# Kernel tuning notes

Hardware: AMD Instinct MI355X
Metric: run time of the kernel (lower is better)

The kernel has to match this reference:

```python
import jax, jax.numpy as jnp
import numpy as np

NUM_CELLS = 15        # num_beams (polar bins over (-pi/2, pi/2])
NEIGH = 2.0           # neighborhood_size -> default fallback radius
P, B = 2048, 10000    # pedestrians, boundary points
EMB, HDIM, MID, BOT = 64, 64, 512, 1024


def setup_inputs() -> dict:
    key = jax.random.key(0)
    ks = jax.random.split(key, 8)
    def n(k, shp, s=1.0):
        return jax.random.normal(k, shp, dtype=jnp.float32) * s
    return {
        "h_states": n(ks[0], (1, P, HDIM)),
        "end_pos": n(ks[1], (P, 2), 4.0),
        "rel_pos": n(ks[2], (P, 2)),
        "boundary_points": n(ks[3], (B, 2), 5.0),
        "W_sp": n(ks[4], (2, EMB), 0.5),
        "b_sp": jnp.zeros((EMB,), jnp.float32),
        "W1": n(ks[5], (EMB + HDIM, MID), 0.05),
        "b1": jnp.zeros((MID,), jnp.float32),
        "g1": jnp.ones((MID,), jnp.float32),
        "be1": jnp.zeros((MID,), jnp.float32),
        "W2": n(ks[6], (MID, BOT), 0.05),
        "b2": jnp.zeros((BOT,), jnp.float32),
        "g2": jnp.ones((BOT,), jnp.float32),
        "be2": jnp.zeros((BOT,), jnp.float32),
    }


def _bn(x, g, b, eps=1e-5):
    # torch BatchNorm1d in training mode: biased batch statistics
    m = x.mean(axis=0)
    v = x.var(axis=0)
    return g * (x - m) * jax.lax.rsqrt(v + eps) + b


def _polar_grid(end_pos, rel_pos, bpts, nb, radius):
    # Vectorized replacement of the pandas pd.cut + groupby(...).idxmin path.
    Pn, Bn = end_pos.shape[0], bpts.shape[0]
    th_ped = jnp.arctan2(rel_pos[:, 1], rel_pos[:, 0])      # (P,)
    c, s = jnp.cos(th_ped)[:, None], jnp.sin(th_ped)[:, None]
    d = bpts[None, :, :] - end_pos[:, None, :]              # (P,B,2)
    xb = d[..., 0] * c + d[..., 1] * s                      # rotate into ped frame
    yb = -d[..., 0] * s + d[..., 1] * c
    r = jnp.sqrt(xb * xb + yb * yb)                         # (P,B)
    th = jnp.arctan2(yb, xb)                                # (P,B)

    width = np.pi / nb
    binid = jnp.clip(jnp.floor((th + np.pi / 2) / width).astype(jnp.int32), 0, nb - 1)
    valid = (th > -np.pi / 2) & (th <= np.pi / 2)           # pd.cut: (a, b] intervals
    pid = jnp.arange(Pn, dtype=jnp.int32)[:, None]
    dump = Pn * nb                                          # segment for out-of-range points
    seg = jnp.where(valid, pid * nb + binid, dump)          # (P,B)

    # appended fallback rows: one per (ped, bin) at bin-center angle, radius=neighborhood_size
    centers = jnp.linspace(-np.pi / 2 + np.pi / nb / 2,
                           np.pi / 2 - np.pi / nb / 2, nb).astype(jnp.float32)
    r_all = jnp.concatenate([r.ravel(), jnp.full((Pn * nb,), radius, jnp.float32)])
    th_all = jnp.concatenate([th.ravel(), jnp.tile(centers, Pn)])
    seg_all = jnp.concatenate([seg.ravel(), jnp.arange(Pn * nb, dtype=jnp.int32)])

    ns = Pn * nb + 1
    rmin = jax.ops.segment_min(r_all, seg_all, num_segments=ns)
    # argmin with first-occurrence tie-break (matches pandas idxmin ordering)
    N = r_all.shape[0]
    idx = jnp.arange(N, dtype=jnp.int32)
    cand = jnp.where(r_all <= rmin[seg_all], idx, N)
    arg = jax.ops.segment_min(cand, seg_all, num_segments=ns)[:Pn * nb]

    th_ch = th_all[arg].reshape(Pn, nb)
    r_ch = rmin[:Pn * nb].reshape(Pn, nb)
    xc = r_ch * jnp.cos(th_ch)
    yc = r_ch * jnp.sin(th_ch)
    # rotate back to world frame and translate
    x = xc * c - yc * s + end_pos[:, 0:1]
    y = xc * s + yc * c + end_pos[:, 1:2]
    return jnp.stack([x, y], axis=-1)                       # (P, nb, 2)


def reference(h_states, end_pos, rel_pos, boundary_points,
              W_sp, b_sp, W1, b1, g1, be1, W2, b2, g2, be2):
    cart = _polar_grid(end_pos, rel_pos, boundary_points, NUM_CELLS, NEIGH)
    rel_grid = (cart - end_pos[:, None, :]).reshape(-1, 2)  # (P*nb, 2)
    emb = rel_grid @ W_sp + b_sp                            # spatial_embedding
    h = h_states.reshape(-1, HDIM)                          # (P, h_dim)
    hid = jnp.repeat(h, NUM_CELLS, axis=0)                  # R1,R1,...,R2,R2,...
    x = jnp.concatenate([emb, hid], axis=1)                 # (P*nb, 128)
    x = jax.nn.relu(_bn(x @ W1 + b1, g1, be1))
    x = jax.nn.relu(_bn(x @ W2 + b2, g2, be2))
    return x.reshape(P, NUM_CELLS, BOT).max(axis=1)         # (P, bottleneck_dim)
```

## Files before the change

### kernel.cpp

```cpp
#include <hip/hip_runtime.h>
#include <hip/hip_bf16.h>
#include <math.h>

#define P_N   2048
#define B_N   10000
#define NB    15
#define MROWS (P_N * NB)
#define SPLIT 5
#define BPB   (B_N / SPLIT)

typedef __bf16 bf16x8 __attribute__((ext_vector_type(8)));
typedef float  f32x4  __attribute__((ext_vector_type(4)));

__device__ __forceinline__ float bf2f(unsigned short u) {
    union { unsigned int i; float f; } v; v.i = ((unsigned int)u) << 16; return v.f;
}
__device__ __forceinline__ unsigned short f2bf(float f) {
    union { float f; unsigned int i; } v; v.f = f;
    unsigned int i = v.i;
    i += 0x7FFFu + ((i >> 16) & 1u);
    return (unsigned short)(i >> 16);
}
__device__ __forceinline__ void gld_lds16(const unsigned short* g, unsigned short* l) {
    __builtin_amdgcn_global_load_lds(
        (const __attribute__((address_space(1))) unsigned int*)g,
        (__attribute__((address_space(3))) unsigned int*)l, 16, 0, 0);
}
__device__ __forceinline__ unsigned fkey(float f) {
    unsigned b = __float_as_uint(f);
    return (b & 0x80000000u) ? ~b : (b | 0x80000000u);
}
__device__ __forceinline__ float funkey(unsigned key) {
    unsigned b = (key & 0x80000000u) ? (key ^ 0x80000000u) : ~key;
    return __uint_as_float(b);
}

__global__ __launch_bounds__(256) void k_front(const float* __restrict__ W1,
        const float* __restrict__ W2, unsigned short* __restrict__ w1t,
        unsigned short* __restrict__ w2t, float* __restrict__ stats,
        const float* __restrict__ end_pos, const float* __restrict__ rel_pos,
        const float* __restrict__ bpts, unsigned long long* __restrict__ pkeys,
        const float* __restrict__ h, unsigned short* __restrict__ hbf,
        const float* __restrict__ Wsp, const float* __restrict__ bsp,
        const float* __restrict__ b1, float* __restrict__ V0,
        float* __restrict__ V1, float* __restrict__ cvec) {
    __shared__ unsigned short t[64][65];
    __shared__ unsigned long long s_key[NB];
    int blk = blockIdx.x, tid = threadIdx.x;
    if (blk < 144) {
        const float* W; unsigned short* O; int NC, K, tr, tc;
        if (blk < 16) { W = W1; O = w1t; NC = 512; K = 128; tr = blk & 1; tc = blk >> 1; }
        else { int b = blk - 16; W = W2; O = w2t; NC = 1024; K = 512; tr = b & 7; tc = b >> 3; }
        int r0 = tr * 64, c0 = tc * 64;
        int cx = tid & 63, rg = tid >> 6;
#pragma unroll
        for (int i = 0; i < 16; ++i) {
            int r = rg * 16 + i;
            t[r][cx] = f2bf(W[(size_t)(r0 + r) * NC + c0 + cx]);
        }
        __syncthreads();
#pragma unroll
        for (int i = 0; i < 16; ++i) {
            int n = rg * 16 + i;
            O[(size_t)(c0 + n) * K + r0 + cx] = t[cx][n];
        }
    } else if (blk < 2196) {
        int zidx = (blk - 144) * 256 + tid;
        if (zidx < 525056) {
            uint4 z = {0u, 0u, 0u, 0u};
            ((uint4*)stats)[zidx] = z;
        }
    } else if (blk < 2198) {
        int col = (blk - 2196) * 256 + tid;
        float v0 = 0.f, v1 = 0.f, cc = 0.f;
        for (int e = 0; e < 64; ++e) {
            float w = W1[(size_t)e * 512 + col];
            v0 = fmaf(Wsp[e], w, v0);
            v1 = fmaf(Wsp[64 + e], w, v1);
            cc = fmaf(bsp[e], w, cc);
        }
        V0[col] = v0; V1[col] = v1; cvec[col] = cc + b1[col];
    } else if (blk < 2326) {
        int base = (blk - 2198) * 1024 + tid * 4;
        float4 hv = *(const float4*)(h + base);
        unsigned short ub[4] = {f2bf(hv.x), f2bf(hv.y), f2bf(hv.z), f2bf(hv.w)};
        *(uint2*)(hbf + base) = *(uint2*)ub;
    } else {
        int sb = blk - 2326;
        int p = sb / SPLIT, part = sb % SPLIT;
        if (tid < NB) s_key[tid] = ~0ull;
        __syncthreads();

        float ex = end_pos[2 * p], ey = end_pos[2 * p + 1];
        float rx = rel_pos[2 * p], ry = rel_pos[2 * p + 1];
        float rr = rx * rx + ry * ry;
        float c, s;
        if (rr > 0.0f) { float inv = 1.0f / sqrtf(rr); c = rx * inv; s = ry * inv; }
        else           { c = 1.0f; s = 0.0f; }

        const float T0 = -4.704630109f, T1 = -2.246036774f, T2 = -1.376381920f,
                    T3 = -0.900404044f, T4 = -0.577350269f, T5 = -0.324919696f,
                    T6 = -0.105104235f, T7 =  0.105104235f, T8 =  0.324919696f,
                    T9 =  0.577350269f, T10 = 0.900404044f, T11 = 1.376381920f,
                    T12 = 2.246036774f, T13 = 4.704630109f;

        const float2* bp2 = (const float2*)bpts;
        int bstart = part * BPB;
        for (int b = bstart + tid; b < bstart + BPB; b += 256) {
            float2 pt = bp2[b];
            float dx = pt.x - ex, dy = pt.y - ey;
            float xb = dx * c + dy * s;
            float yb = dy * c - dx * s;
            float r2 = xb * xb + yb * yb;
            bool v3 = yb > T7 * xb;
            float ta = v3 ? T11 : T3;
            bool v2 = yb > ta * xb;
            float tb = v3 ? (v2 ? T13 : T9) : (v2 ? T5 : T1);
            bool v1 = yb > tb * xb;
            float tc = v3 ? (v2 ? (v1 ? 3.0e38f : T12) : (v1 ? T10 : T8))
                          : (v2 ? (v1 ? T6 : T4)       : (v1 ? T2 : T0));
            bool v0 = yb > tc * xb;
            int bin = (v3 ? 8 : 0) + (v2 ? 4 : 0) + (v1 ? 2 : 0) + (v0 ? 1 : 0);
            if (xb > 0.0f) {
                unsigned long long key =
                    ((unsigned long long)__float_as_uint(r2) << 32) | (unsigned int)b;
                atomicMin(&s_key[bin], key);
            }
        }
        __syncthreads();
        if (tid < NB) pkeys[(size_t)part * MROWS + p * NB + tid] = s_key[tid];
    }
}

__global__ __launch_bounds__(64) void k_assemble(
        const unsigned long long* __restrict__ pkeys,
        const float* __restrict__ end_pos, const float* __restrict__ rel_pos,
        const float* __restrict__ bpts, float* __restrict__ rel,
        float* __restrict__ pm0, float* __restrict__ pm1, float* __restrict__ pm2,
        float* __restrict__ pm3, float* __restrict__ pm4) {
    int p = blockIdx.x, tid = threadIdx.x;
    float relx = 0.f, rely = 0.f;
    if (tid < NB) {
        float ex = end_pos[2 * p], ey = end_pos[2 * p + 1];
        unsigned long long key = ~0ull;
#pragma unroll
        for (int part = 0; part < SPLIT; ++part) {
            unsigned long long k = pkeys[(size_t)part * MROWS + p * NB + tid];
            key = (k < key) ? k : key;
        }
        float r = sqrtf(__uint_as_float((unsigned int)(key >> 32)));
        if (r <= 2.0f) {
            int b = (int)(key & 0xFFFFFFFFu);
            relx = bpts[2 * b] - ex; rely = bpts[2 * b + 1] - ey;
        } else {
            float rx = rel_pos[2 * p], ry = rel_pos[2 * p + 1];
            float rr = rx * rx + ry * ry;
            float c, s;
            if (rr > 0.0f) { float inv = 1.0f / sqrtf(rr); c = rx * inv; s = ry * inv; }
            else           { c = 1.0f; s = 0.0f; }
            float th = ((float)tid + 0.5f) * (float)(M_PI / 15.0) - (float)(M_PI / 2.0);
            float xc = 2.0f * cosf(th), yc = 2.0f * sinf(th);
            relx = xc * c - yc * s;
            rely = xc * s + yc * c;
        }
        rel[(size_t)(p * NB + tid) * 2]     = relx;
        rel[(size_t)(p * NB + tid) * 2 + 1] = rely;
    }
    float m0 = relx, m1 = rely, m2 = relx * relx, m3 = relx * rely, m4 = rely * rely;
#pragma unroll
    for (int d = 32; d >= 1; d >>= 1) {
        m0 += __shfl_xor(m0, d); m1 += __shfl_xor(m1, d);
        m2 += __shfl_xor(m2, d); m3 += __shfl_xor(m3, d);
        m4 += __shfl_xor(m4, d);
    }
    if (tid == 0) { pm0[p] = m0; pm1[p] = m1; pm2[p] = m2; pm3[p] = m3; pm4[p] = m4; }
}

__global__ __launch_bounds__(512) void k_hgemm(const unsigned short* __restrict__ hbf,
        const unsigned short* __restrict__ w1t, float* __restrict__ Hp,
        const float* __restrict__ V0, const float* __restrict__ V1,
        const float* __restrict__ cvec,
        const float* __restrict__ pm0, const float* __restrict__ pm1,
        const float* __restrict__ pm2, const float* __restrict__ pm3,
        const float* __restrict__ pm4,
        float* __restrict__ s1, float* __restrict__ q1) {
    __shared__ __align__(16) unsigned short lds[24576];
    int tid = threadIdx.x;
    int bm = blockIdx.x & 15, bnn = blockIdx.x >> 4;
    int row0 = bm << 7, col0 = bnn << 8;
    int lane = tid & 63, wave = tid >> 6;
    int wr = wave >> 2, wc = wave & 3;
    int frow = lane & 15, kq = lane >> 4;

    f32x4 zero = {0.f, 0.f, 0.f, 0.f};
    f32x4 acc[4][4];
#pragma unroll
    for (int i = 0; i < 4; ++i)
#pragma unroll
        for (int j = 0; j < 4; ++j) acc[i][j] = zero;

#pragma unroll
    for (int k = 0; k < 6; ++k) {
        int ch = wave * 6 + k;
        int s = (ch >= 24) ? 1 : 0;
        int r = ch - s * 24;
        unsigned short* dst = lds + s * 12288 + r * 512;
        const unsigned short* src =
            (r < 8) ? (hbf + (size_t)(row0 + r * 16 + frow) * 64 + s * 32 + kq * 8)
                    : (w1t + (size_t)(col0 + (r - 8) * 16 + frow) * 128 + 64 + s * 32 + kq * 8);
        gld_lds16(src, dst);
    }
    asm volatile("s_waitcnt vmcnt(0)" ::: "memory");
    __builtin_amdgcn_s_barrier();
    asm volatile("" ::: "memory");

#pragma unroll
    for (int s = 0; s < 2; ++s) {
        const unsigned short* sub = lds + s * 12288;
        bf16x8 af[4], bfv[4];
#pragma unroll
        for (int i = 0; i < 4; ++i)
            af[i] = *(const bf16x8*)&sub[(wr * 4 + i) * 512 + kq * 128 + frow * 8];
#pragma unroll
        for (int j = 0; j < 4; ++j)
            bfv[j] = *(const bf16x8*)&sub[4096 + (wc * 4 + j) * 512 + kq * 128 + frow * 8];
#pragma unroll
        for (int i = 0; i < 4; ++i)
#pragma unroll
            for (int j = 0; j < 4; ++j)
                acc[i][j] = __builtin_amdgcn_mfma_f32_16x16x32_bf16(af[i], bfv[j], acc[i][j], 0, 0, 0);
    }

    float v0c[4], v1c[4], cc[4];
#pragma unroll
    for (int j = 0; j < 4; ++j) {
        int col = col0 + wc * 64 + j * 16 + frow;
        v0c[j] = V0[col]; v1c[j] = V1[col]; cc[j] = cvec[col];
    }
    float csum[4] = {0.f, 0.f, 0.f, 0.f}, csq[4] = {0.f, 0.f, 0.f, 0.f};
#pragma unroll
    for (int i = 0; i < 4; ++i) {
#pragma unroll
        for (int r = 0; r < 4; ++r) {
            int row = row0 + wr * 64 + i * 16 + kq * 4 + r;
            float srx = pm0[row], sry = pm1[row];
            float sxx = pm2[row], sxy = pm3[row], syy = pm4[row];
#pragma unroll
            for (int j = 0; j < 4; ++j) {
                int col = col0 + wc * 64 + j * 16 + frow;
                float hp = acc[i][j][r];
                Hp[(size_t)row * 512 + col] = hp;
                float A  = hp + cc[j];
                float B1 = fmaf(srx, v0c[j], sry * v1c[j]);
                float B2 = fmaf(v0c[j] * v0c[j], sxx,
                           fmaf(2.0f * v0c[j] * v1c[j], sxy, v1c[j] * v1c[j] * syy));
                csum[j] += fmaf(15.0f, A, B1);
                csq[j]  += fmaf(15.0f, A * A, fmaf(2.0f * A, B1, B2));
            }
        }
    }
#pragma unroll
    for (int j = 0; j < 4; ++j) {
        int col = col0 + wc * 64 + j * 16 + frow;
        float cs = csum[j], cq = csq[j];
        cs += __shfl_xor(cs, 16); cs += __shfl_xor(cs, 32);
        cq += __shfl_xor(cq, 16); cq += __shfl_xor(cq, 32);
        if (lane < 16) { atomicAdd(&s1[col], cs); atomicAdd(&q1[col], cq); }
    }
}

__global__ __launch_bounds__(256) void k_y1w(const float* __restrict__ Hp,
        const float* __restrict__ rel, const float* __restrict__ V0,
        const float* __restrict__ V1, const float* __restrict__ cvec,
        const float* __restrict__ s1, const float* __restrict__ q1,
        const float* __restrict__ g1, const float* __restrict__ be1,
        unsigned short* __restrict__ Y1) {
    int tid = threadIdx.x;
    int p = blockIdx.x;
    int seg = tid & 63, cg = tid >> 6;
    const float invN = 1.0f / (float)MROWS;
    float4 ha = *(const float4*)(Hp + (size_t)p * 512 + seg * 8);
    float4 hb = *(const float4*)(Hp + (size_t)p * 512 + seg * 8 + 4);
    float4 ca = *(const float4*)(cvec + seg * 8);
    float4 cb = *(const float4*)(cvec + seg * 8 + 4);
    float4 va = *(const float4*)(V0 + seg * 8), vb = *(const float4*)(V0 + seg * 8 + 4);
    float4 wa = *(const float4*)(V1 + seg * 8), wb = *(const float4*)(V1 + seg * 8 + 4);
    float hc[8] = {ha.x+ca.x, ha.y+ca.y, ha.z+ca.z, ha.w+ca.w,
                   hb.x+cb.x, hb.y+cb.y, hb.z+cb.z, hb.w+cb.w};
    float v0[8] = {va.x,va.y,va.z,va.w,vb.x,vb.y,vb.z,vb.w};
    float v1[8] = {wa.x,wa.y,wa.z,wa.w,wb.x,wb.y,wb.z,wb.w};
    float sc[8], sh[8];
#pragma unroll
    for (int j = 0; j < 8; ++j) {
        int ccix = seg * 8 + j;
        float m = s1[ccix] * invN;
        float v = q1[ccix] * invN - m * m;
        float k = g1[ccix] * rsqrtf(v + 1e-5f);
        sc[j] = k; sh[j] = be1[ccix] - m * k;
    }
#pragma unroll
    for (int i = 0; i < 4; ++i) {
        int cell = cg + i * 4;
        if (cell < NB) {
            float2 rl = *(const float2*)(rel + (size_t)(p * NB + cell) * 2);
            unsigned short ub[8];
#pragma unroll
            for (int j = 0; j < 8; ++j) {
                float y = fmaf(rl.x, v0[j], fmaf(rl.y, v1[j], hc[j]));
                float z = fmaxf(fmaf(y, sc[j], sh[j]), 0.0f);
                ub[j] = f2bf(z);
            }
            *(uint4*)(Y1 + (size_t)(p * NB + cell) * 512 + seg * 8) = *(uint4*)ub;
        }
    }
}

template<int K, bool WRITE_C>
__global__ __launch_bounds__(512) void k_gemm256(
        const unsigned short* __restrict__ A, const unsigned short* __restrict__ Bt,
        const float* __restrict__ bias, unsigned short* __restrict__ C,
        int N, float* __restrict__ osum, float* __restrict__ osq,
        unsigned int* __restrict__ mkey) {
    __shared__ __align__(16) unsigned short lds[65536];
    int tid = threadIdx.x;

    int nbt = N >> 8;
    int d = blockIdx.x;
    int m5 = d >> 3;
    int bn = m5 % nbt;
    int bm = (d & 7) + ((m5 / nbt) << 3);
    int row0 = bm << 8, col0 = bn << 8;

    int lane = tid & 63, wave = tid >> 6;
    int wr = wave >> 2, wc = wave & 3;
    int frow = lane & 15, kq = lane >> 4;

    f32x4 zero = {0.f, 0.f, 0.f, 0.f};
    f32x4 acc[8][4];
#pragma unroll
    for (int i = 0; i < 8; ++i)
#pragma unroll
        for (int j = 0; j < 4; ++j) acc[i][j] = zero;

    const unsigned short* gsrc =
        (wave < 4) ? (A  + (size_t)(row0 + (wave << 6) + frow) * K + kq * 8)
                   : (Bt + (size_t)(col0 + ((wave - 4) << 6) + frow) * K + kq * 8);
    unsigned regbase = (wave < 4) ? (unsigned)wave * 2048
                                  : 8192u + (unsigned)(wave - 4) * 2048;

    auto issue2 = [&](int t, int s, int hp) {
        unsigned short* dst = lds + (t & 1) * 32768 + s * 16384 + regbase + hp * 1024;
        const unsigned short* src = gsrc + t * 64 + s * 32 + (size_t)(hp * 32) * K;
        gld_lds16(src,                  dst);
        gld_lds16(src + (size_t)16 * K, dst + 512);
    };

    constexpr int NT = K / 64;
    static_assert(NT >= 2, "need >=2 K-tiles");

    issue2(0, 0, 0); issue2(0, 0, 1); issue2(0, 1, 0); issue2(0, 1, 1);

#pragma unroll
    for (int t = 0; t < NT; ++t) {
        const unsigned short* buf = lds + (t & 1) * 32768;
        bool more = (t + 1 < NT);
#pragma unroll
        for (int s = 0; s < 2; ++s) {
            const unsigned short* sub = buf + s * 16384;
            if (more || s == 0) asm volatile("s_waitcnt vmcnt(4)" ::: "memory");
            else                asm volatile("s_waitcnt vmcnt(0)" ::: "memory");
            __builtin_amdgcn_s_barrier();
            asm volatile("" ::: "memory");
            bf16x8 bfv[4], af[4];
#pragma unroll
            for (int j = 0; j < 4; ++j)
                bfv[j] = *(const bf16x8*)&sub[8192 + (wc * 4 + j) * 512 + kq * 128 + frow * 8];
#pragma unroll
            for (int i = 0; i < 4; ++i)
                af[i] = *(const bf16x8*)&sub[(wr * 8 + i) * 512 + kq * 128 + frow * 8];
            if (more) issue2(t + 1, s, 0);
            __builtin_amdgcn_s_barrier();
            asm volatile("" ::: "memory");
            __builtin_amdgcn_s_setprio(1);
#pragma unroll
            for (int i = 0; i < 4; ++i)
#pragma unroll
                for (int j = 0; j < 4; ++j)
                    acc[i][j] = __builtin_amdgcn_mfma_f32_16x16x32_bf16(af[i], bfv[j], acc[i][j], 0, 0, 0);
            __builtin_amdgcn_s_setprio(0);
#pragma unroll
            for (int i = 0; i < 4; ++i)
                af[i] = *(const bf16x8*)&sub[(wr * 8 + 4 + i) * 512 + kq * 128 + frow * 8];
            if (more) issue2(t + 1, s, 1);
            __builtin_amdgcn_s_barrier();
            asm volatile("" ::: "memory");
            __builtin_amdgcn_s_setprio(1);
#pragma unroll
            for (int i = 0; i < 4; ++i)
#pragma unroll
                for (int j = 0; j < 4; ++j)
                    acc[4 + i][j] = __builtin_amdgcn_mfma_f32_16x16x32_bf16(af[i], bfv[j], acc[4 + i][j], 0, 0, 0);
            __builtin_amdgcn_s_setprio(0);
        }
    }

    float bv[4];
#pragma unroll
    for (int j = 0; j < 4; ++j) bv[j] = bias[col0 + wc * 64 + j * 16 + frow];

#pragma unroll
    for (int j = 0; j < 4; ++j) {
        int col = col0 + wc * 64 + j * 16 + frow;
        float csum = 0.f, csq = 0.f;
#pragma unroll
        for (int i = 0; i < 8; ++i) {
#pragma unroll
            for (int r = 0; r < 4; ++r) {
                float y = acc[i][j][r] + bv[j];
                csum += y; csq = fmaf(y, y, csq);
            }
        }
        csum += __shfl_xor(csum, 16); csum += __shfl_xor(csum, 32);
        csq  += __shfl_xor(csq, 16);  csq  += __shfl_xor(csq, 32);
        if (lane < 16) { atomicAdd(&osum[col], csum); atomicAdd(&osq[col], csq); }
    }

    unsigned short* ldsC = lds;
#pragma unroll
    for (int b = 0; b < 4; ++b) {
        __syncthreads();
        if (wr == (b >> 1)) {
#pragma unroll
            for (int j = 0; j < 4; ++j) {
#pragma unroll
                for (int ii = 0; ii < 4; ++ii) {
                    int i = (b & 1) * 4 + ii;
#pragma unroll
                    for (int r = 0; r < 4; ++r) {
                        float y = acc[i][j][r] + bv[j];
                        ldsC[(ii * 16 + kq * 4 + r) * 264 + wc * 64 + j * 16 + frow] = f2bf(y);
                    }
                }
            }
        }
        __syncthreads();
        if (WRITE_C) {
#pragma unroll
            for (int it = 0; it < 4; ++it) {
                int s = it * 512 + tid;
                int brow = s >> 5, seg = s & 31;
                *(uint4*)(C + (size_t)(row0 + b * 64 + brow) * N + col0 + seg * 8) =
                    *(const uint4*)&ldsC[brow * 264 + seg * 8];
            }
        } else {
            int col = tid & 255, half = tid >> 8;
            int lrow0 = half * 32;
            int grow = row0 + b * 64 + lrow0;
            int curp = grow / 15;
            int rem = 15 - (grow - curp * 15);
            float mx = -3.0e38f;
#pragma unroll
            for (int r = 0; r < 32; ++r) {
                mx = fmaxf(mx, bf2f(ldsC[(lrow0 + r) * 264 + col]));
                if (--rem == 0) {
                    atomicMax(&mkey[(size_t)curp * 1024 + col0 + col], fkey(mx));
                    mx = -3.0e38f; ++curp; rem = 15;
                }
            }
            if (rem != 15)
                atomicMax(&mkey[(size_t)curp * 1024 + col0 + col], fkey(mx));
        }
    }
}

__global__ void k_bnfin(const unsigned int* __restrict__ mkey, const float* __restrict__ s2,
                        const float* __restrict__ q2, const float* __restrict__ g2,
                        const float* __restrict__ be2, float* __restrict__ out) {
    int idx = blockIdx.x * 256 + threadIdx.x;
    int p = idx >> 7, cb = idx & 127;
    int c0 = cb << 3;
    const float invN = 1.0f / (float)MROWS;
    float4 sa = *(const float4*)(s2 + c0),  sb = *(const float4*)(s2 + c0 + 4);
    float4 qa = *(const float4*)(q2 + c0),  qb = *(const float4*)(q2 + c0 + 4);
    float4 ga = *(const float4*)(g2 + c0),  gb = *(const float4*)(g2 + c0 + 4);
    float4 ea = *(const float4*)(be2 + c0), eb = *(const float4*)(be2 + c0 + 4);
    float sv[8] = {sa.x,sa.y,sa.z,sa.w,sb.x,sb.y,sb.z,sb.w};
    float qv[8] = {qa.x,qa.y,qa.z,qa.w,qb.x,qb.y,qb.z,qb.w};
    float gv[8] = {ga.x,ga.y,ga.z,ga.w,gb.x,gb.y,gb.z,gb.w};
    float ev[8] = {ea.x,ea.y,ea.z,ea.w,eb.x,eb.y,eb.z,eb.w};
    uint4 k0 = *(const uint4*)(mkey + (size_t)p * 1024 + c0);
    uint4 k1 = *(const uint4*)(mkey + (size_t)p * 1024 + c0 + 4);
    unsigned kv[8] = {k0.x,k0.y,k0.z,k0.w,k1.x,k1.y,k1.z,k1.w};
    float o[8];
#pragma unroll
    for (int j = 0; j < 8; ++j) {
        float m = sv[j] * invN;
        float v = qv[j] * invN - m * m;
        float k = gv[j] * rsqrtf(v + 1e-5f);
        float sh = ev[j] - m * k;
        o[j] = fmaxf(fmaf(funkey(kv[j]), k, sh), 0.0f);
    }
    float4 o0 = {o[0], o[1], o[2], o[3]};
    float4 o1 = {o[4], o[5], o[6], o[7]};
    *(float4*)(out + (size_t)p * 1024 + c0)     = o0;
    *(float4*)(out + (size_t)p * 1024 + c0 + 4) = o1;
}

extern "C" void kernel_launch(void* const* d_in, const int* in_sizes, int n_in,
                              void* d_out, int out_size, void* d_ws, size_t ws_size,
                              hipStream_t stream) {
    const float* h       = (const float*)d_in[0];
    const float* end_pos = (const float*)d_in[1];
    const float* rel_pos = (const float*)d_in[2];
    const float* bpts    = (const float*)d_in[3];
    const float* Wsp     = (const float*)d_in[4];
    const float* bsp     = (const float*)d_in[5];
    const float* W1      = (const float*)d_in[6];
    const float* b1      = (const float*)d_in[7];
    const float* g1      = (const float*)d_in[8];
    const float* be1     = (const float*)d_in[9];
    const float* W2      = (const float*)d_in[10];
    const float* b2      = (const float*)d_in[11];
    const float* g2      = (const float*)d_in[12];
    const float* be2     = (const float*)d_in[13];
    float* out = (float*)d_out;

    char* ws = (char*)d_ws;
    float* s1  = (float*)ws;
    float* q1  = s1 + 512;
    float* s2  = q1 + 512;
    float* q2  = s2 + 1024;
    unsigned int* mkey        = (unsigned int*)(ws + 12288);
    unsigned long long* pkeys = (unsigned long long*)(ws + 12288 + 8388608);
    unsigned short* w1t = (unsigned short*)(ws + 9629696);
    unsigned short* w2t = (unsigned short*)(ws + 9760768);
    unsigned short* hbf = (unsigned short*)(ws + 10809344);
    float* V0   = (float*)(ws + 11071488);
    float* V1   = V0 + 512;
    float* cvec = V1 + 512;
    float* Hp   = (float*)(ws + 11081728);
    float* rel  = (float*)(ws + 15276032);
    unsigned short* Y1 = (unsigned short*)(ws + 15521792);
    float* pm0 = (float*)(ws + 46979072);
    float* pm1 = pm0 + 2048;
    float* pm2 = pm1 + 2048;
    float* pm3 = pm2 + 2048;
    float* pm4 = pm3 + 2048;

    k_front<<<12566, 256, 0, stream>>>(W1, W2, w1t, w2t, s1, end_pos, rel_pos,
                                       bpts, pkeys, h, hbf, Wsp, bsp, b1, V0, V1, cvec);
    k_assemble<<<P_N, 64, 0, stream>>>(pkeys, end_pos, rel_pos, bpts, rel,
                                       pm0, pm1, pm2, pm3, pm4);
    k_hgemm<<<32, 512, 0, stream>>>(hbf, w1t, Hp, V0, V1, cvec,
                                    pm0, pm1, pm2, pm3, pm4, s1, q1);
    k_y1w<<<P_N, 256, 0, stream>>>(Hp, rel, V0, V1, cvec, s1, q1, g1, be1, Y1);
    k_gemm256<512, false><<<(MROWS / 256) * (1024 / 256), 512, 0, stream>>>(
        Y1, w2t, b2, nullptr, 1024, s2, q2, mkey);
    k_bnfin<<<(P_N * 128) / 256, 256, 0, stream>>>(mkey, s2, q2, g2, be2, out);
}
```

Before: 116.3 us.

## Batch four pedestrians per block and cull boundary points beyond the neighborhood radius

The polar-grid search blocks now each handle four pedestrians, so every loaded boundary point is reused four times and the grid shrinks accordingly. Points are also rejected early when their squared distance exceeds the neighborhood radius squared (with a small tolerance), so the rotation, bin search and shared-memory atomicMin are skipped for most points. This cuts ALU work and LDS atomic contention. It relies on out-of-radius points never being chosen, which the assemble step's default-radius fallback is assumed to cover, and it lowers the number of blocks in flight.

Result: faster. 111.8 us (median of 3 runs) (-3.9%).

```diff
diff --git a/kernel.cpp b/kernel.cpp
--- a/kernel.cpp
+++ b/kernel.cpp
@@ -45,7 +45,7 @@
         const float* __restrict__ b1, float* __restrict__ V0,
         float* __restrict__ V1, float* __restrict__ cvec) {
     __shared__ unsigned short t[64][65];
-    __shared__ unsigned long long s_key[NB];
+    __shared__ unsigned long long s_key[4][16];
     int blk = blockIdx.x, tid = threadIdx.x;
     if (blk < 144) {
         const float* W; unsigned short* O; int NC, K, tr, tc;
@@ -87,16 +87,21 @@
         *(uint2*)(hbf + base) = *(uint2*)ub;
     } else {
         int sb = blk - 2326;
-        int p = sb / SPLIT, part = sb % SPLIT;
-        if (tid < NB) s_key[tid] = ~0ull;
+        int pg = sb / SPLIT, part = sb % SPLIT;
+        int p0 = pg * 4;
+        if (tid < 64) s_key[tid >> 4][tid & 15] = ~0ull;
         __syncthreads();
 
-        float ex = end_pos[2 * p], ey = end_pos[2 * p + 1];
-        float rx = rel_pos[2 * p], ry = rel_pos[2 * p + 1];
-        float rr = rx * rx + ry * ry;
-        float c, s;
-        if (rr > 0.0f) { float inv = 1.0f / sqrtf(rr); c = rx * inv; s = ry * inv; }
-        else           { c = 1.0f; s = 0.0f; }
+        float ex[4], ey[4], cr[4], sr[4];
+#pragma unroll
+        for (int pi = 0; pi < 4; ++pi) {
+            ex[pi] = end_pos[2 * (p0 + pi)];
+            ey[pi] = end_pos[2 * (p0 + pi) + 1];
+            float rx = rel_pos[2 * (p0 + pi)], ry = rel_pos[2 * (p0 + pi) + 1];
+            float rr = rx * rx + ry * ry;
+            if (rr > 0.0f) { float inv = 1.0f / sqrtf(rr); cr[pi] = rx * inv; sr[pi] = ry * inv; }
+            else           { cr[pi] = 1.0f; sr[pi] = 0.0f; }
+        }
 
         const float T0 = -4.704630109f, T1 = -2.246036774f, T2 = -1.376381920f,
                     T3 = -0.900404044f, T4 = -0.577350269f, T5 = -0.324919696f,
@@ -108,27 +113,36 @@
         int bstart = part * BPB;
         for (int b = bstart + tid; b < bstart + BPB; b += 256) {
             float2 pt = bp2[b];
-            float dx = pt.x - ex, dy = pt.y - ey;
-            float xb = dx * c + dy * s;
-            float yb = dy * c - dx * s;
-            float r2 = xb * xb + yb * yb;
-            bool v3 = yb > T7 * xb;
-            float ta = v3 ? T11 : T3;
-            bool v2 = yb > ta * xb;
-            float tb = v3 ? (v2 ? T13 : T9) : (v2 ? T5 : T1);
-            bool v1 = yb > tb * xb;
-            float tc = v3 ? (v2 ? (v1 ? 3.0e38f : T12) : (v1 ? T10 : T8))
-                          : (v2 ? (v1 ? T6 : T4)       : (v1 ? T2 : T0));
-            bool v0 = yb > tc * xb;
-            int bin = (v3 ? 8 : 0) + (v2 ? 4 : 0) + (v1 ? 2 : 0) + (v0 ? 1 : 0);
-            if (xb > 0.0f) {
-                unsigned long long key =
-                    ((unsigned long long)__float_as_uint(r2) << 32) | (unsigned int)b;
-                atomicMin(&s_key[bin], key);
+#pragma unroll
+            for (int pi = 0; pi < 4; ++pi) {
+                float dx = pt.x - ex[pi], dy = pt.y - ey[pi];
+                float r2u = fmaf(dx, dx, dy * dy);
+                if (r2u <= 4.0001f) {
+                    float c = cr[pi], s = sr[pi];
+                    float xb = dx * c + dy * s;
+                    float yb = dy * c - dx * s;
+                    if (xb > 0.0f) {
+                        float r2 = fmaf(xb, xb, yb * yb);
+                        bool v3 = yb > T7 * xb;
+                        float ta = v3 ? T11 : T3;
+                        bool v2 = yb > ta * xb;
+                        float tb = v3 ? (v2 ? T13 : T9) : (v2 ? T5 : T1);
+                        bool v1 = yb > tb * xb;
+                        float tc = v3 ? (v2 ? (v1 ? 3.0e38f : T12) : (v1 ? T10 : T8))
+                                      : (v2 ? (v1 ? T6 : T4)       : (v1 ? T2 : T0));
+                        bool v0 = yb > tc * xb;
+                        int bin = (v3 ? 8 : 0) + (v2 ? 4 : 0) + (v1 ? 2 : 0) + (v0 ? 1 : 0);
+                        unsigned long long key =
+                            ((unsigned long long)__float_as_uint(r2) << 32) | (unsigned int)b;
+                        atomicMin(&s_key[pi][bin], key);
+                    }
+                }
             }
         }
         __syncthreads();
-        if (tid < NB) pkeys[(size_t)part * MROWS + p * NB + tid] = s_key[tid];
+        if (tid < 64 && (tid & 15) < NB)
+            pkeys[(size_t)part * MROWS + (p0 + (tid >> 4)) * NB + (tid & 15)] =
+                s_key[tid >> 4][tid & 15];
     }
 }
 
@@ -547,8 +561,8 @@
     float* pm3 = pm2 + 2048;
     float* pm4 = pm3 + 2048;
 
-    k_front<<<12566, 256, 0, stream>>>(W1, W2, w1t, w2t, s1, end_pos, rel_pos,
-                                       bpts, pkeys, h, hbf, Wsp, bsp, b1, V0, V1, cvec);
+    k_front<<<4886, 256, 0, stream>>>(W1, W2, w1t, w2t, s1, end_pos, rel_pos,
+                                      bpts, pkeys, h, hbf, Wsp, bsp, b1, V0, V1, cvec);
     k_assemble<<<P_N, 64, 0, stream>>>(pkeys, end_pos, rel_pos, bpts, rel,
                                        pm0, pm1, pm2, pm3, pm4);
     k_hgemm<<<32, 512, 0, stream>>>(hbf, w1t, Hp, V0, V1, cvec,
```
